# Optimization experiments

Hardware: AMD Instinct MI355X
Metric: run time of the kernel (lower is better)

The kernel has to match this reference:

```python
import jax, jax.numpy as jnp
import numpy as np

B, S, D, K, F = 4, 2048, 1024, 4, 4096
C_COEF = 8.0  # RG-LRU gating exponent from Griffin paper
EPS = 1e-6


def setup_inputs() -> dict:
    key = jax.random.key(0)
    ks = jax.random.split(key, 12)
    def n(k, shape, scale=1.0):
        return jax.random.normal(k, shape, dtype=jnp.float32) * scale
    sd = 1.0 / np.sqrt(D)
    return {
        "x": n(ks[0], (B, S, D)),
        "velocity": n(ks[1], (B, S, D), 0.1),
        "pre_norm_w": jnp.ones((D,), jnp.float32),
        "conv_kernel": n(ks[2], (D, K), 0.3),   # depthwise causal conv weights
        "conv_bias": jnp.zeros((D,), jnp.float32),
        "W_gate": n(ks[3], (D, D), sd),
        "W_a": n(ks[4], (D, D), sd),
        "lam": n(ks[5], (D,)),
        "W_out": n(ks[6], (2 * D, D), 1.0 / np.sqrt(2 * D)),
        "b_out": jnp.zeros((D,), jnp.float32),
        "log_beta": n(ks[7], (D,), 0.5),
        "ffn_norm_w": jnp.ones((D,), jnp.float32),
        "W_ff1": n(ks[8], (D, F), sd),
        "b_ff1": jnp.zeros((F,), jnp.float32),
        "W_ff2": n(ks[9], (F, D), 1.0 / np.sqrt(F)),
        "b_ff2": jnp.zeros((D,), jnp.float32),
    }


def _rmsnorm(x, w):
    # matches: rsqrt(x.float().pow(2).mean(-1, keepdim=True) + 1e-6); cast back; * weight
    xf = x.astype(jnp.float32)
    rms = jax.lax.rsqrt(jnp.mean(xf * xf, axis=-1, keepdims=True) + EPS)
    return (xf * rms).astype(x.dtype) * w


def _causal_dwconv(x, kernel, bias):
    # y[b,t,d] = bias[d] + sum_k kernel[d,k] * x[b,t-k,d]  (causal depthwise)
    k_taps = kernel.shape[1]
    s = x.shape[1]
    pad = jnp.pad(x, ((0, 0), (k_taps - 1, 0), (0, 0)))
    out = bias
    for k in range(k_taps):  # tiny fixed loop over kernel taps
        out = out + pad[:, k_taps - 1 - k : k_taps - 1 - k + s, :] * kernel[:, k]
    return out


def _griffin_scan(x, W_gate, W_a, lam):
    # RG-LRU: h_t = a_t * h_{t-1} + sqrt(1 - a_t^2) * (i_t * x_t)
    gate = jax.nn.sigmoid(jnp.einsum("bsd,de->bse", x, W_gate))
    log_a = -C_COEF * jax.nn.softplus(lam) * jax.nn.sigmoid(
        jnp.einsum("bsd,de->bse", x, W_a)
    )  # [B,S,D], log_a <= 0
    a = jnp.exp(log_a)
    u = jnp.sqrt(jnp.maximum(1.0 - a * a, 0.0)) * (gate * x)

    def step(h, au):
        a_t, u_t = au
        h = a_t * h + u_t
        return h, h

    a_t = jnp.moveaxis(a, 1, 0)  # [S,B,D]
    u_t = jnp.moveaxis(u, 1, 0)
    h0 = jnp.zeros_like(a_t[0])
    _, hs = jax.lax.scan(step, h0, (a_t, u_t))
    return jnp.moveaxis(hs, 0, 1)  # [B,S,D]


def reference(x, velocity, pre_norm_w, conv_kernel, conv_bias, W_gate, W_a, lam,
              W_out, b_out, log_beta, ffn_norm_w, W_ff1, b_ff1, W_ff2, b_ff2):
    x_norm = _rmsnorm(x, pre_norm_w)
    conv_out = _causal_dwconv(x_norm, conv_kernel, conv_bias)
    griffin_out = _griffin_scan(x_norm, W_gate, W_a, lam)
    mixer_out = jnp.concatenate([conv_out, griffin_out], axis=-1) @ W_out + b_out
    beta = jax.nn.sigmoid(log_beta)
    velocity = beta * velocity + mixer_out
    x = x + velocity
    normed = _rmsnorm(x, ffn_norm_w)
    ffn = jax.nn.gelu(normed @ W_ff1 + b_ff1) @ W_ff2 + b_ff2
    return (x + ffn, velocity)
```

## Files before the change

kernel.cpp:

```cpp
#include <hip/hip_runtime.h>

static constexpr int Bb = 4;
static constexpr int Ss = 2048;
static constexpr int Dd = 1024;
static constexpr int Ff = 4096;
static constexpr int Mm = Bb * Ss;
static constexpr size_t ND = (size_t)Mm * Dd;
static constexpr int CH = 32;
static constexpr int CL = Ss / CH;

typedef __attribute__((ext_vector_type(8))) short short8;
typedef __attribute__((ext_vector_type(4))) float floatx4;

__device__ __forceinline__ unsigned f2bf(float f) {
  unsigned u = __builtin_bit_cast(unsigned, f);
  return (u + 0x7FFFu + ((u >> 16) & 1u)) >> 16;
}
__device__ __forceinline__ float bf2f(unsigned bits) {
  return __builtin_bit_cast(float, bits << 16);
}
__device__ __forceinline__ void gload_lds16(const void* g, void* lds) {
  __builtin_amdgcn_global_load_lds((const __attribute__((address_space(1))) void*)g,
                                   (__attribute__((address_space(3))) void*)lds,
                                   16, 0, 0);
}

__global__ __launch_bounds__(256) void wconv_k(const float* __restrict__ W,
                                               unsigned short* __restrict__ WT,
                                               int K, int N) {
  __shared__ float tile[32][33];
  int tx = threadIdx.x & 31, ty = threadIdx.x >> 5;
  int bx = blockIdx.x * 32, by = blockIdx.y * 32;
#pragma unroll
  for (int i = 0; i < 32; i += 8)
    tile[ty + i][tx] = W[(size_t)(by + ty + i) * N + bx + tx];
  __syncthreads();
#pragma unroll
  for (int i = 0; i < 32; i += 8)
    WT[(size_t)(bx + ty + i) * K + by + tx] = (unsigned short)f2bf(tile[tx][ty + i]);
}

__global__ __launch_bounds__(256) void rmsnorm_bf_k(const float* __restrict__ x,
                                                    const float* __restrict__ w,
                                                    unsigned short* __restrict__ out) {
  int row = blockIdx.x;
  const float4* xr = (const float4*)(x + (size_t)row * Dd);
  int t = threadIdx.x;
  float4 v = xr[t];
  float ss = v.x * v.x + v.y * v.y + v.z * v.z + v.w * v.w;
#pragma unroll
  for (int off = 32; off > 0; off >>= 1) ss += __shfl_down(ss, off, 64);
  __shared__ float sb[4];
  if ((t & 63) == 0) sb[t >> 6] = ss;
  __syncthreads();
  float tot = sb[0] + sb[1] + sb[2] + sb[3];
  float sc = rsqrtf(tot * (1.0f / (float)Dd) + 1e-6f);
  float4 wv = ((const float4*)w)[t];
  unsigned lo = f2bf(v.x * sc * wv.x) | (f2bf(v.y * sc * wv.y) << 16);
  unsigned hi = f2bf(v.z * sc * wv.z) | (f2bf(v.w * sc * wv.w) << 16);
  *(uint2*)(out + (size_t)row * Dd + t * 4) = make_uint2(lo, hi);
}

__global__ __launch_bounds__(256) void conv_k(const unsigned short* __restrict__ xn,
                                              const float* __restrict__ kern,
                                              const float* __restrict__ bias,
                                              unsigned short* __restrict__ outC) {
  size_t q = (size_t)blockIdx.x * 256 + threadIdx.x;
  size_t i = q * 4;
  int d = (int)(i & (Dd - 1));
  int m = (int)(i >> 10);
  int t = m & (Ss - 1);
  float acc[4];
#pragma unroll
  for (int j = 0; j < 4; j++) acc[j] = bias[d + j];
#pragma unroll
  for (int k = 0; k < 4; k++) {
    if (t >= k) {
      uint2 xv = *(const uint2*)(xn + i - (size_t)k * Dd);
      float x0 = bf2f(xv.x & 0xFFFF), x1 = bf2f(xv.x >> 16);
      float x2 = bf2f(xv.y & 0xFFFF), x3 = bf2f(xv.y >> 16);
      acc[0] = fmaf(kern[(d + 0) * 4 + k], x0, acc[0]);
      acc[1] = fmaf(kern[(d + 1) * 4 + k], x1, acc[1]);
      acc[2] = fmaf(kern[(d + 2) * 4 + k], x2, acc[2]);
      acc[3] = fmaf(kern[(d + 3) * 4 + k], x3, acc[3]);
    }
  }
  unsigned lo = f2bf(acc[0]) | (f2bf(acc[1]) << 16);
  unsigned hi = f2bf(acc[2]) | (f2bf(acc[3]) << 16);
  *(uint2*)(outC + (size_t)m * (2 * Dd) + d) = make_uint2(lo, hi);
}

template <int MODE>
__global__ __launch_bounds__(256) void bgemm_k(const unsigned short* __restrict__ A,
                                               const unsigned short* __restrict__ BT,
                                               void* __restrict__ Cout,
                                               int M, int N, int K,
                                               const float* __restrict__ bias,
                                               const float* __restrict__ extra,
                                               const float* __restrict__ vel_in,
                                               const float* __restrict__ x_in,
                                               const float* __restrict__ log_beta,
                                               float* __restrict__ vel_out) {
  __shared__ unsigned short As[128 * 32];
  __shared__ unsigned short Bs[128 * 32];
  const int tid = threadIdx.x;
  const int wave = tid >> 6, lane = tid & 63;
  const int r = lane & 15, quad = lane >> 4;
  const int wm = wave >> 1, wn = wave & 1;
  const int bm = blockIdx.y * 128, bn = blockIdx.x * 128;

  const unsigned short* Ab = A + (size_t)bm * K;
  const unsigned short* Bp = BT + (size_t)bn * K;
  const int srow = 32 * wave + (lane >> 2);
  const int scol = (lane & 3) * 8;

  floatx4 acc[4][4];
#pragma unroll
  for (int i = 0; i < 4; i++)
#pragma unroll
    for (int j = 0; j < 4; j++) acc[i][j] = (floatx4){0.f, 0.f, 0.f, 0.f};

  for (int k0 = 0; k0 < K; k0 += 32) {
    __syncthreads();
    gload_lds16(Ab + (size_t)srow * K + k0 + scol,        As + wave * 1024);
    gload_lds16(Ab + (size_t)(srow + 16) * K + k0 + scol, As + wave * 1024 + 512);
    gload_lds16(Bp + (size_t)srow * K + k0 + scol,        Bs + wave * 1024);
    gload_lds16(Bp + (size_t)(srow + 16) * K + k0 + scol, Bs + wave * 1024 + 512);
    __syncthreads();
    short8 af[4], bfr[4];
#pragma unroll
    for (int i = 0; i < 4; i++)
      af[i] = *(const short8*)&As[(wm * 64 + i * 16 + r) * 32 + quad * 8];
#pragma unroll
    for (int j = 0; j < 4; j++)
      bfr[j] = *(const short8*)&Bs[(wn * 64 + j * 16 + r) * 32 + quad * 8];
#pragma unroll
    for (int i = 0; i < 4; i++)
#pragma unroll
      for (int j = 0; j < 4; j++)
        acc[i][j] = __builtin_amdgcn_mfma_f32_16x16x32_bf16(af[i], bfr[j], acc[i][j], 0, 0, 0);
  }

#pragma unroll
  for (int i = 0; i < 4; i++) {
#pragma unroll
    for (int j = 0; j < 4; j++) {
      int colg = bn + wn * 64 + j * 16 + r;
      float bv = (MODE & 1) ? bias[colg] : 0.0f;
      float beta = (MODE & 16) ? 1.0f / (1.0f + expf(-log_beta[colg])) : 0.0f;
#pragma unroll
      for (int reg = 0; reg < 4; reg++) {
        int rowg = bm + wm * 64 + i * 16 + quad * 4 + reg;
        size_t idx = (size_t)rowg * N + colg;
        float v = acc[i][j][reg] + bv;
        if (MODE & 2) {
          float c = v + 0.044715f * v * v * v;
          v = 0.5f * v * (1.0f + tanhf(0.7978845608028654f * c));
        }
        if (MODE & 4) v += extra[idx];
        if (MODE & 16) {
          float vn = fmaf(beta, vel_in[idx], v);
          vel_out[idx] = vn;
          v = x_in[idx] + vn;
        }
        if (MODE & 8)
          ((unsigned short*)Cout)[idx] = (unsigned short)f2bf(v);
        else
          ((float*)Cout)[idx] = v;
      }
    }
  }
}

__global__ __launch_bounds__(256) void scan_p1(const unsigned short* __restrict__ gpre,
                                               const unsigned short* __restrict__ apre,
                                               const unsigned short* __restrict__ xn,
                                               const float* __restrict__ lam,
                                               unsigned short* __restrict__ ub,
                                               float* __restrict__ carryA,
                                               float* __restrict__ carryH) {
  int g = blockIdx.x * 256 + threadIdx.x;
  int e = g & (Dd - 1);
  int bc = g >> 10;
  int b = bc & 3;
  int c = bc >> 2;
  float l = lam[e];
  float sp = fmaxf(l, 0.0f) + log1pf(expf(-fabsf(l)));
  float m8sp = -8.0f * sp;
  size_t base = ((size_t)b * Ss + (size_t)c * CL) * Dd + e;
  float A = 1.0f, h = 0.0f;
#pragma unroll 4
  for (int t = 0; t < CL; t++) {
    size_t idx = base + (size_t)t * Dd;
    float ap = bf2f(apre[idx]);
    float gp = bf2f(gpre[idx]);
    float xv = bf2f(xn[idx]);
    float sa = 1.0f / (1.0f + expf(-ap));
    float a = expf(m8sp * sa);
    float gg = 1.0f / (1.0f + expf(-gp));
    float u = sqrtf(fmaxf(1.0f - a * a, 0.0f)) * gg * xv;
    ub[idx] = (unsigned short)f2bf(u);
    A *= a;
    h = fmaf(a, h, u);
  }
  carryA[c * 4096 + b * 1024 + e] = A;
  carryH[c * 4096 + b * 1024 + e] = h;
}

__global__ __launch_bounds__(256) void scan_p2(const float* __restrict__ carryA,
                                               const float* __restrict__ carryH,
                                               float* __restrict__ init) {
  int ch = blockIdx.x * 256 + threadIdx.x;
  float H = 0.0f;
#pragma unroll
  for (int c = 0; c < CH; c++) {
    init[c * 4096 + ch] = H;
    H = fmaf(carryA[c * 4096 + ch], H, carryH[c * 4096 + ch]);
  }
}

__global__ __launch_bounds__(256) void scan_p3(const unsigned short* __restrict__ apre,
                                               const unsigned short* __restrict__ ub,
                                               const float* __restrict__ lam,
                                               const float* __restrict__ init,
                                               unsigned short* __restrict__ outC) {
  int g = blockIdx.x * 256 + threadIdx.x;
  int e = g & (Dd - 1);
  int bc = g >> 10;
  int b = bc & 3;
  int c = bc >> 2;
  float l = lam[e];
  float sp = fmaxf(l, 0.0f) + log1pf(expf(-fabsf(l)));
  float m8sp = -8.0f * sp;
  size_t base = ((size_t)b * Ss + (size_t)c * CL) * Dd + e;
  size_t ob = ((size_t)b * Ss + (size_t)c * CL) * (2 * Dd) + Dd + e;
  float h = init[c * 4096 + b * 1024 + e];
#pragma unroll 4
  for (int t = 0; t < CL; t++) {
    size_t idx = base + (size_t)t * Dd;
    float ap = bf2f(apre[idx]);
    float sa = 1.0f / (1.0f + expf(-ap));
    float a = expf(m8sp * sa);
    float u = bf2f(ub[idx]);
    h = fmaf(a, h, u);
    outC[ob + (size_t)t * (2 * Dd)] = (unsigned short)f2bf(h);
  }
}

extern "C" void kernel_launch(void* const* d_in, const int* in_sizes, int n_in,
                              void* d_out, int out_size, void* d_ws, size_t ws_size,
                              hipStream_t stream) {
  const float* x        = (const float*)d_in[0];
  const float* velocity = (const float*)d_in[1];
  const float* pre_w    = (const float*)d_in[2];
  const float* conv_w   = (const float*)d_in[3];
  const float* conv_b   = (const float*)d_in[4];
  const float* W_gate   = (const float*)d_in[5];
  const float* W_a      = (const float*)d_in[6];
  const float* lam      = (const float*)d_in[7];
  const float* W_out    = (const float*)d_in[8];
  const float* b_out    = (const float*)d_in[9];
  const float* log_beta = (const float*)d_in[10];
  const float* ffn_w    = (const float*)d_in[11];
  const float* W_ff1    = (const float*)d_in[12];
  const float* b_ff1    = (const float*)d_in[13];
  const float* W_ff2    = (const float*)d_in[14];
  const float* b_ff2    = (const float*)d_in[15];

  float* out0 = (float*)d_out;
  float* out1 = out0 + ND;

  const size_t MB = 1024 * 1024;
  char* ws = (char*)d_ws;
  unsigned short* WgT   = (unsigned short*)ws;
  unsigned short* WaT   = WgT + (size_t)1024 * 1024;
  unsigned short* WoT   = WaT + (size_t)1024 * 1024;
  unsigned short* Wf1T  = WoT + (size_t)2 * 1024 * 1024;
  unsigned short* Wf2T  = Wf1T + (size_t)4 * 1024 * 1024;
  float*          mixer = (float*)(ws + 24 * MB);
  float*          carA  = (float*)(ws + 24 * MB);
  float*          carH  = (float*)(ws + 24 * MB + 512 * 1024);
  float*          initb = (float*)(ws + 25 * MB);
  unsigned short* conc  = (unsigned short*)(ws + 56 * MB);
  unsigned short* gpre  = (unsigned short*)(ws + 88 * MB);
  unsigned short* apre  = (unsigned short*)(ws + 104 * MB);
  unsigned short* xnbf  = (unsigned short*)(ws + 120 * MB);
  unsigned short* ubf   = (unsigned short*)(ws + 136 * MB);
  unsigned short* midbf = (unsigned short*)(ws + 88 * MB);
  unsigned short* nrmbf = (unsigned short*)(ws + 56 * MB);

  const int EB = 256;
  const int egrid4 = (int)(ND / 4 / EB);

  wconv_k<<<dim3(32, 32),  256, 0, stream>>>(W_gate, WgT, 1024, 1024);
  wconv_k<<<dim3(32, 32),  256, 0, stream>>>(W_a,    WaT, 1024, 1024);
  wconv_k<<<dim3(32, 64),  256, 0, stream>>>(W_out,  WoT, 2048, 1024);
  wconv_k<<<dim3(128, 32), 256, 0, stream>>>(W_ff1,  Wf1T, 1024, 4096);
  wconv_k<<<dim3(32, 128), 256, 0, stream>>>(W_ff2,  Wf2T, 4096, 1024);
  rmsnorm_bf_k<<<Mm, 256, 0, stream>>>(x, pre_w, xnbf);
  conv_k<<<egrid4, EB, 0, stream>>>(xnbf, conv_w, conv_b, conc);
  bgemm_k<8><<<dim3(8, 64), 256, 0, stream>>>(xnbf, WgT, gpre, Mm, 1024, 1024,
      nullptr, nullptr, nullptr, nullptr, nullptr, nullptr);
  bgemm_k<8><<<dim3(8, 64), 256, 0, stream>>>(xnbf, WaT, apre, Mm, 1024, 1024,
      nullptr, nullptr, nullptr, nullptr, nullptr, nullptr);
  scan_p1<<<512, 256, 0, stream>>>(gpre, apre, xnbf, lam, ubf, carA, carH);
  scan_p2<<<16, 256, 0, stream>>>(carA, carH, initb);
  scan_p3<<<512, 256, 0, stream>>>(apre, ubf, lam, initb, conc);
  bgemm_k<1 | 16><<<dim3(8, 64), 256, 0, stream>>>(conc, WoT, mixer, Mm, 1024, 2048,
      b_out, nullptr, velocity, x, log_beta, out1);
  rmsnorm_bf_k<<<Mm, 256, 0, stream>>>(mixer, ffn_w, nrmbf);
  bgemm_k<1 | 2 | 8><<<dim3(32, 64), 256, 0, stream>>>(nrmbf, Wf1T, midbf, Mm, 4096, 1024,
      b_ff1, nullptr, nullptr, nullptr, nullptr, nullptr);
  bgemm_k<1 | 4><<<dim3(8, 64), 256, 0, stream>>>(midbf, Wf2T, out0, Mm, 1024, 4096,
      b_ff2, mixer, nullptr, nullptr, nullptr, nullptr);
}
```

Measured before the change: 662.2 us.

## Swizzle GEMM LDS, swap MFMA operands for vector epilogue, fuse gate/a GEMMs

```diff
diff --git a/kernel.cpp b/kernel.cpp
--- a/kernel.cpp
+++ b/kernel.cpp
@@ -112,7 +112,8 @@
   const unsigned short* Ab = A + (size_t)bm * K;
   const unsigned short* Bp = BT + (size_t)bn * K;
   const int srow = 32 * wave + (lane >> 2);
-  const int scol = (lane & 3) * 8;
+  const int scol = (((lane & 3) ^ ((lane >> 4) & 3))) * 8;
+  const int kcA = (quad ^ ((r >> 2) & 3)) * 8;
 
   floatx4 acc[4][4];
 #pragma unroll
@@ -130,50 +131,69 @@
     short8 af[4], bfr[4];
 #pragma unroll
     for (int i = 0; i < 4; i++)
-      af[i] = *(const short8*)&As[(wm * 64 + i * 16 + r) * 32 + quad * 8];
+      af[i] = *(const short8*)&As[(wm * 64 + i * 16 + r) * 32 + kcA];
 #pragma unroll
     for (int j = 0; j < 4; j++)
-      bfr[j] = *(const short8*)&Bs[(wn * 64 + j * 16 + r) * 32 + quad * 8];
+      bfr[j] = *(const short8*)&Bs[(wn * 64 + j * 16 + r) * 32 + kcA];
 #pragma unroll
     for (int i = 0; i < 4; i++)
 #pragma unroll
       for (int j = 0; j < 4; j++)
-        acc[i][j] = __builtin_amdgcn_mfma_f32_16x16x32_bf16(af[i], bfr[j], acc[i][j], 0, 0, 0);
+        acc[i][j] = __builtin_amdgcn_mfma_f32_16x16x32_bf16(bfr[j], af[i], acc[i][j], 0, 0, 0);
   }
 
 #pragma unroll
   for (int i = 0; i < 4; i++) {
+    int rowg = bm + wm * 64 + i * 16 + r;
 #pragma unroll
     for (int j = 0; j < 4; j++) {
-      int colg = bn + wn * 64 + j * 16 + r;
-      float bv = (MODE & 1) ? bias[colg] : 0.0f;
-      float beta = (MODE & 16) ? 1.0f / (1.0f + expf(-log_beta[colg])) : 0.0f;
-#pragma unroll
-      for (int reg = 0; reg < 4; reg++) {
-        int rowg = bm + wm * 64 + i * 16 + quad * 4 + reg;
-        size_t idx = (size_t)rowg * N + colg;
-        float v = acc[i][j][reg] + bv;
-        if (MODE & 2) {
+      int colg = bn + wn * 64 + j * 16 + quad * 4;
+      size_t idx = (size_t)rowg * N + colg;
+      float v0 = acc[i][j][0], v1 = acc[i][j][1], v2 = acc[i][j][2], v3 = acc[i][j][3];
+      if (MODE & 1) {
+        float4 bv = *(const float4*)(bias + colg);
+        v0 += bv.x; v1 += bv.y; v2 += bv.z; v3 += bv.w;
+      }
+      if (MODE & 2) {
+        float vv[4] = {v0, v1, v2, v3};
+#pragma unroll
+        for (int q2 = 0; q2 < 4; q2++) {
+          float v = vv[q2];
           float c = v + 0.044715f * v * v * v;
-          v = 0.5f * v * (1.0f + tanhf(0.7978845608028654f * c));
+          vv[q2] = 0.5f * v * (1.0f + tanhf(0.7978845608028654f * c));
         }
-        if (MODE & 4) v += extra[idx];
-        if (MODE & 16) {
-          float vn = fmaf(beta, vel_in[idx], v);
-          vel_out[idx] = vn;
-          v = x_in[idx] + vn;
-        }
-        if (MODE & 8)
-          ((unsigned short*)Cout)[idx] = (unsigned short)f2bf(v);
-        else
-          ((float*)Cout)[idx] = v;
+        v0 = vv[0]; v1 = vv[1]; v2 = vv[2]; v3 = vv[3];
+      }
+      if (MODE & 4) {
+        float4 ev = *(const float4*)(extra + idx);
+        v0 += ev.x; v1 += ev.y; v2 += ev.z; v3 += ev.w;
+      }
+      if (MODE & 16) {
+        float4 lb = *(const float4*)(log_beta + colg);
+        float4 vi = *(const float4*)(vel_in + idx);
+        float4 xi = *(const float4*)(x_in + idx);
+        float4 vn;
+        vn.x = fmaf(1.0f / (1.0f + expf(-lb.x)), vi.x, v0);
+        vn.y = fmaf(1.0f / (1.0f + expf(-lb.y)), vi.y, v1);
+        vn.z = fmaf(1.0f / (1.0f + expf(-lb.z)), vi.z, v2);
+        vn.w = fmaf(1.0f / (1.0f + expf(-lb.w)), vi.w, v3);
+        *(float4*)(vel_out + idx) = vn;
+        v0 = xi.x + vn.x; v1 = xi.y + vn.y; v2 = xi.z + vn.z; v3 = xi.w + vn.w;
+      }
+      if (MODE & 8) {
+        uint2 pk;
+        pk.x = f2bf(v0) | (f2bf(v1) << 16);
+        pk.y = f2bf(v2) | (f2bf(v3) << 16);
+        *(uint2*)((unsigned short*)Cout + idx) = pk;
+      } else {
+        float4 o; o.x = v0; o.y = v1; o.z = v2; o.w = v3;
+        *(float4*)((float*)Cout + idx) = o;
       }
     }
   }
 }
 
-__global__ __launch_bounds__(256) void scan_p1(const unsigned short* __restrict__ gpre,
-                                               const unsigned short* __restrict__ apre,
+__global__ __launch_bounds__(256) void scan_p1(const unsigned short* __restrict__ gapre,
                                                const unsigned short* __restrict__ xn,
                                                const float* __restrict__ lam,
                                                unsigned short* __restrict__ ub,
@@ -187,19 +207,19 @@
   float l = lam[e];
   float sp = fmaxf(l, 0.0f) + log1pf(expf(-fabsf(l)));
   float m8sp = -8.0f * sp;
-  size_t base = ((size_t)b * Ss + (size_t)c * CL) * Dd + e;
+  size_t m0 = (size_t)b * Ss + (size_t)c * CL;
   float A = 1.0f, h = 0.0f;
 #pragma unroll 4
   for (int t = 0; t < CL; t++) {
-    size_t idx = base + (size_t)t * Dd;
-    float ap = bf2f(apre[idx]);
-    float gp = bf2f(gpre[idx]);
-    float xv = bf2f(xn[idx]);
+    size_t m = m0 + t;
+    float gp = bf2f(gapre[m * 2048 + e]);
+    float ap = bf2f(gapre[m * 2048 + 1024 + e]);
+    float xv = bf2f(xn[m * Dd + e]);
     float sa = 1.0f / (1.0f + expf(-ap));
     float a = expf(m8sp * sa);
     float gg = 1.0f / (1.0f + expf(-gp));
     float u = sqrtf(fmaxf(1.0f - a * a, 0.0f)) * gg * xv;
-    ub[idx] = (unsigned short)f2bf(u);
+    ub[m * Dd + e] = (unsigned short)f2bf(u);
     A *= a;
     h = fmaf(a, h, u);
   }
@@ -219,7 +239,7 @@
   }
 }
 
-__global__ __launch_bounds__(256) void scan_p3(const unsigned short* __restrict__ apre,
+__global__ __launch_bounds__(256) void scan_p3(const unsigned short* __restrict__ gapre,
                                                const unsigned short* __restrict__ ub,
                                                const float* __restrict__ lam,
                                                const float* __restrict__ init,
@@ -232,18 +252,17 @@
   float l = lam[e];
   float sp = fmaxf(l, 0.0f) + log1pf(expf(-fabsf(l)));
   float m8sp = -8.0f * sp;
-  size_t base = ((size_t)b * Ss + (size_t)c * CL) * Dd + e;
-  size_t ob = ((size_t)b * Ss + (size_t)c * CL) * (2 * Dd) + Dd + e;
+  size_t m0 = (size_t)b * Ss + (size_t)c * CL;
   float h = init[c * 4096 + b * 1024 + e];
 #pragma unroll 4
   for (int t = 0; t < CL; t++) {
-    size_t idx = base + (size_t)t * Dd;
-    float ap = bf2f(apre[idx]);
+    size_t m = m0 + t;
+    float ap = bf2f(gapre[m * 2048 + 1024 + e]);
     float sa = 1.0f / (1.0f + expf(-ap));
     float a = expf(m8sp * sa);
-    float u = bf2f(ub[idx]);
+    float u = bf2f(ub[m * Dd + e]);
     h = fmaf(a, h, u);
-    outC[ob + (size_t)t * (2 * Dd)] = (unsigned short)f2bf(h);
+    outC[m * (2 * Dd) + Dd + e] = (unsigned short)f2bf(h);
   }
 }
 
@@ -272,9 +291,8 @@
 
   const size_t MB = 1024 * 1024;
   char* ws = (char*)d_ws;
-  unsigned short* WgT   = (unsigned short*)ws;
-  unsigned short* WaT   = WgT + (size_t)1024 * 1024;
-  unsigned short* WoT   = WaT + (size_t)1024 * 1024;
+  unsigned short* WgaT  = (unsigned short*)ws;
+  unsigned short* WoT   = WgaT + (size_t)2 * 1024 * 1024;
   unsigned short* Wf1T  = WoT + (size_t)2 * 1024 * 1024;
   unsigned short* Wf2T  = Wf1T + (size_t)4 * 1024 * 1024;
   float*          mixer = (float*)(ws + 24 * MB);
@@ -282,8 +300,7 @@
   float*          carH  = (float*)(ws + 24 * MB + 512 * 1024);
   float*          initb = (float*)(ws + 25 * MB);
   unsigned short* conc  = (unsigned short*)(ws + 56 * MB);
-  unsigned short* gpre  = (unsigned short*)(ws + 88 * MB);
-  unsigned short* apre  = (unsigned short*)(ws + 104 * MB);
+  unsigned short* gapre = (unsigned short*)(ws + 88 * MB);
   unsigned short* xnbf  = (unsigned short*)(ws + 120 * MB);
   unsigned short* ubf   = (unsigned short*)(ws + 136 * MB);
   unsigned short* midbf = (unsigned short*)(ws + 88 * MB);
@@ -292,20 +309,18 @@
   const int EB = 256;
   const int egrid4 = (int)(ND / 4 / EB);
 
-  wconv_k<<<dim3(32, 32),  256, 0, stream>>>(W_gate, WgT, 1024, 1024);
-  wconv_k<<<dim3(32, 32),  256, 0, stream>>>(W_a,    WaT, 1024, 1024);
+  wconv_k<<<dim3(32, 32),  256, 0, stream>>>(W_gate, WgaT, 1024, 1024);
+  wconv_k<<<dim3(32, 32),  256, 0, stream>>>(W_a,    WgaT + (size_t)1024 * 1024, 1024, 1024);
   wconv_k<<<dim3(32, 64),  256, 0, stream>>>(W_out,  WoT, 2048, 1024);
   wconv_k<<<dim3(128, 32), 256, 0, stream>>>(W_ff1,  Wf1T, 1024, 4096);
   wconv_k<<<dim3(32, 128), 256, 0, stream>>>(W_ff2,  Wf2T, 4096, 1024);
   rmsnorm_bf_k<<<Mm, 256, 0, stream>>>(x, pre_w, xnbf);
   conv_k<<<egrid4, EB, 0, stream>>>(xnbf, conv_w, conv_b, conc);
-  bgemm_k<8><<<dim3(8, 64), 256, 0, stream>>>(xnbf, WgT, gpre, Mm, 1024, 1024,
+  bgemm_k<8><<<dim3(16, 64), 256, 0, stream>>>(xnbf, WgaT, gapre, Mm, 2048, 1024,
       nullptr, nullptr, nullptr, nullptr, nullptr, nullptr);
-  bgemm_k<8><<<dim3(8, 64), 256, 0, stream>>>(xnbf, WaT, apre, Mm, 1024, 1024,
-      nullptr, nullptr, nullptr, nullptr, nullptr, nullptr);
-  scan_p1<<<512, 256, 0, stream>>>(gpre, apre, xnbf, lam, ubf, carA, carH);
+  scan_p1<<<512, 256, 0, stream>>>(gapre, xnbf, lam, ubf, carA, carH);
   scan_p2<<<16, 256, 0, stream>>>(carA, carH, initb);
-  scan_p3<<<512, 256, 0, stream>>>(apre, ubf, lam, initb, conc);
+  scan_p3<<<512, 256, 0, stream>>>(gapre, ubf, lam, initb, conc);
   bgemm_k<1 | 16><<<dim3(8, 64), 256, 0, stream>>>(conc, WoT, mixer, Mm, 1024, 2048,
       b_out, nullptr, velocity, x, log_beta, out1);
   rmsnorm_bf_k<<<Mm, 256, 0, stream>>>(mixer, ffn_w, nrmbf);
```

Result: no change. 664.6 us (+0.4%).
